# Performance work log

Hardware: AMD Instinct MI355X
Metric: run time of the kernel (lower is better)

The kernel has to match this reference:

```python
import jax, jax.numpy as jnp
import numpy as np

D = 1024   # n_embd
H = 16     # n_head
HD = D // H

def setup_inputs() -> dict:
    key = jax.random.key(0)
    ks = jax.random.split(key, 6)
    s = 1.0 / np.sqrt(D)
    x  = jax.random.normal(ks[0], (4, 2048, D), dtype=jnp.float32)
    Wq = jax.random.uniform(ks[1], (D, D), jnp.float32, -s, s)
    Wk = jax.random.uniform(ks[2], (D, D), jnp.float32, -s, s)
    Wv = jax.random.uniform(ks[3], (D, D), jnp.float32, -s, s)
    Wp = jax.random.uniform(ks[4], (D, D), jnp.float32, -s, s)
    bp = jax.random.uniform(ks[5], (D,),   jnp.float32, -s, s)
    return {"x": x, "Wq": Wq, "Wk": Wk, "Wv": Wv, "Wp": Wp, "bp": bp}

def reference(x, Wq, Wk, Wv, Wp, bp):
    B, T, C = x.shape
    scale = 1.0 / np.sqrt(HD)
    # torch nn.Linear: y = x @ W.T
    q = (x @ Wq.T).reshape(B, T, H, HD).transpose(0, 2, 1, 3)  # [B,H,T,hd]
    k = (x @ Wk.T).reshape(B, T, H, HD).transpose(0, 2, 1, 3)
    v = (x @ Wv.T).reshape(B, T, H, HD).transpose(0, 2, 1, 3)
    att = jnp.einsum('bhqd,bhkd->bhqk', q, k) * scale           # [B,H,T,T]
    causal = jnp.tril(jnp.ones((T, T), dtype=bool))
    att = jnp.where(causal[None, None], att, -jnp.inf)
    att = jax.nn.softmax(att, axis=-1)
    y = jnp.einsum('bhqk,bhkd->bhqd', att, v)                   # [B,H,T,hd]
    y = y.transpose(0, 2, 1, 3).reshape(B, T, C)
    return y @ Wp.T + bp
```

## Files before the change

kernel.cpp:

```cpp
#include <hip/hip_runtime.h>
#include <hip/hip_bf16.h>
#include <math.h>


#define B_  4
#define T_  2048
#define D_  1024
#define H_  16
#define HD_ 64
#define M_  (B_ * T_)

typedef short bf16x8 __attribute__((ext_vector_type(8)));
typedef float f32x4  __attribute__((ext_vector_type(4)));

__device__ __forceinline__ f32x4 mfma16(bf16x8 a, bf16x8 b, f32x4 c) {
    return __builtin_amdgcn_mfma_f32_16x16x32_bf16(a, b, c, 0, 0, 0);
}

__device__ __forceinline__ void gl_lds16(const unsigned short* g, unsigned short* l) {
    __builtin_amdgcn_global_load_lds(
        (const __attribute__((address_space(1))) void*)g,
        (__attribute__((address_space(3))) void*)l, 16, 0, 0);
}

__device__ __forceinline__ unsigned short f2bf(float f) {
    union { __hip_bfloat16 h; unsigned short u; } cv;
    cv.h = __float2bfloat16(f);
    return cv.u;
}
__device__ __forceinline__ float bf2f(unsigned short u) {
    return __uint_as_float(((unsigned)u) << 16);
}
__device__ __forceinline__ float exp2_fast(float x) {
    return __builtin_amdgcn_exp2f(x);
}

struct su4 { unsigned short x, y, z, w; };

__global__ __launch_bounds__(256)
void cvt_kernel(const float* __restrict__ in, unsigned short* __restrict__ out) {
    const int i = blockIdx.x * 256 + threadIdx.x;
    const float4 v = ((const float4*)in)[i];
    su4 o;
    o.x = f2bf(v.x); o.y = f2bf(v.y); o.z = f2bf(v.z); o.w = f2bf(v.w);
    ((su4*)out)[i] = o;
}

__global__ __launch_bounds__(256)
void cvtw_kernel(const float* __restrict__ w0, const float* __restrict__ w1,
                 const float* __restrict__ w2, const float* __restrict__ w3,
                 unsigned short* __restrict__ o0, unsigned short* __restrict__ o1,
                 unsigned short* __restrict__ o2, unsigned short* __restrict__ o3) {
    const int y = blockIdx.y;
    const float* in       = (y == 0) ? w0 : (y == 1) ? w1 : (y == 2) ? w2 : w3;
    unsigned short* out   = (y == 0) ? o0 : (y == 1) ? o1 : (y == 2) ? o2 : o3;
    const int i = blockIdx.x * 256 + threadIdx.x;
    const float4 v = ((const float4*)in)[i];
    su4 o;
    o.x = f2bf(v.x); o.y = f2bf(v.y); o.z = f2bf(v.z); o.w = f2bf(v.w);
    ((su4*)out)[i] = o;
}

__global__ __launch_bounds__(256, 2)
void qkv_kernel(const unsigned short* __restrict__ X,
                const unsigned short* __restrict__ Wq,
                const unsigned short* __restrict__ Wk,
                const unsigned short* __restrict__ Wv,
                unsigned short* __restrict__ Qo,
                unsigned short* __restrict__ Ko,
                unsigned short* __restrict__ Vo)
{
    __shared__ unsigned short As[128 * 64];
    __shared__ unsigned short Bs[128 * 64];

    const int m0 = blockIdx.x * 128;
    const int by = blockIdx.y;
    const unsigned short* W = (by < 8) ? Wq : (by < 16) ? Wk : Wv;
    unsigned short*       O = (by < 8) ? Qo : (by < 16) ? Ko : Vo;
    const int n0   = (by & 7) * 128;
    const bool vsec = (by >= 16);
    const int tid  = threadIdx.x;
    const int lane = tid & 63;
    const int wv   = tid >> 6;
    const int wr   = (wv >> 1) * 64;
    const int wc   = (wv & 1) * 64;
    const int g    = lane >> 4;
    const int c    = lane & 15;

    f32x4 acc[4][4] = {};

    for (int k0 = 0; k0 < D_; k0 += 64) {
        #pragma unroll
        for (int i = 0; i < 4; ++i) {
            const int flat = i * 2048 + tid * 8;
            const int row = flat >> 6, col = flat & 63;
            gl_lds16(X + (size_t)(m0 + row) * D_ + k0 + col, As + flat);
            gl_lds16(W + (size_t)(n0 + row) * D_ + k0 + col, Bs + flat);
        }
        __syncthreads();
        #pragma unroll
        for (int kk = 0; kk < 64; kk += 32) {
            bf16x8 af[4], bg[4];
            #pragma unroll
            for (int mi = 0; mi < 4; ++mi)
                af[mi] = *(const bf16x8*)(As + (wr + mi * 16 + c) * 64 + kk + g * 8);
            #pragma unroll
            for (int ni = 0; ni < 4; ++ni)
                bg[ni] = *(const bf16x8*)(Bs + (wc + ni * 16 + c) * 64 + kk + g * 8);
            if (!vsec) {
                #pragma unroll
                for (int mi = 0; mi < 4; ++mi)
                    #pragma unroll
                    for (int ni = 0; ni < 4; ++ni)
                        acc[mi][ni] = mfma16(af[mi], bg[ni], acc[mi][ni]);
            } else {
                #pragma unroll
                for (int mi = 0; mi < 4; ++mi)
                    #pragma unroll
                    for (int ni = 0; ni < 4; ++ni)
                        acc[mi][ni] = mfma16(bg[ni], af[mi], acc[mi][ni]);
            }
        }
        __syncthreads();
    }

    if (!vsec) {
        #pragma unroll
        for (int mi = 0; mi < 4; ++mi)
            #pragma unroll
            for (int ni = 0; ni < 4; ++ni)
                #pragma unroll
                for (int r = 0; r < 4; ++r) {
                    const int m = m0 + wr + mi * 16 + g * 4 + r;
                    const int n = n0 + wc + ni * 16 + c;
                    const int b = m >> 11, t = m & (T_ - 1);
                    const int h = n >> 6,  hd = n & 63;
                    O[((size_t)((b << 4) + h) * T_ + t) * HD_ + hd] = f2bf(acc[mi][ni][r]);
                }
    } else {
        #pragma unroll
        for (int mi = 0; mi < 4; ++mi)
            #pragma unroll
            for (int ni = 0; ni < 4; ++ni)
                #pragma unroll
                for (int r = 0; r < 4; ++r) {
                    const int n = n0 + wc + ni * 16 + g * 4 + r;
                    const int m = m0 + wr + mi * 16 + c;
                    const int b = m >> 11, t = m & (T_ - 1);
                    const int h = n >> 6,  hd = n & 63;
                    O[((size_t)((b << 4) + h) * HD_ + hd) * T_ + t] = f2bf(acc[mi][ni][r]);
                }
    }
}

__device__ __forceinline__ bf16x8 ptrans(const f32x4& p0, const f32x4& p1,
                                         int lane, int g, int c) {
    unsigned int P32[2][2];
    P32[0][0] = (unsigned int)f2bf(p0[0]) | ((unsigned int)f2bf(p0[1]) << 16);
    P32[0][1] = (unsigned int)f2bf(p0[2]) | ((unsigned int)f2bf(p0[3]) << 16);
    P32[1][0] = (unsigned int)f2bf(p1[0]) | ((unsigned int)f2bf(p1[1]) << 16);
    P32[1][1] = (unsigned int)f2bf(p1[2]) | ((unsigned int)f2bf(p1[3]) << 16);
    const int sl0 = c + ((lane & 16) << 1);
    const int sl1 = sl0 + 16;
    const int q00 = __shfl((int)P32[0][0], sl0), q10 = __shfl((int)P32[1][0], sl0);
    const int q01 = __shfl((int)P32[0][1], sl0), q11 = __shfl((int)P32[1][1], sl0);
    const int q02 = __shfl((int)P32[0][0], sl1), q12 = __shfl((int)P32[1][0], sl1);
    const int q03 = __shfl((int)P32[0][1], sl1), q13 = __shfl((int)P32[1][1], sl1);
    const bool nhi = (g & 2) != 0;
    union { unsigned int u[4]; bf16x8 v; } pf;
    pf.u[0] = nhi ? q10 : q00;
    pf.u[1] = nhi ? q11 : q01;
    pf.u[2] = nhi ? q12 : q02;
    pf.u[3] = nhi ? q13 : q03;
    return pf.v;
}

__global__ __launch_bounds__(256, 4)
void attn_kernel(const unsigned short* __restrict__ Q,
                 const unsigned short* __restrict__ K,
                 const unsigned short* __restrict__ VT,
                 unsigned short* __restrict__ Y)
{
    __shared__ unsigned short Ks[4096];
    __shared__ unsigned short Vs[4096];

    const int bh = blockIdx.x;
    const int pr = blockIdx.y;
    const unsigned short* Qp  = Q  + (size_t)bh * T_ * HD_;
    const unsigned short* Kp  = K  + (size_t)bh * T_ * HD_;
    const unsigned short* VTp = VT + (size_t)bh * HD_ * T_;
    const int b = bh >> 4, h = bh & 15;

    const int tid  = threadIdx.x;
    const int lane = tid & 63;
    const int w    = tid >> 6;
    const int g    = lane >> 4;
    const int c    = lane & 15;
    const float SC = 0.18033688011112042f;

    int srowK[2], scolK[2];
    #pragma unroll
    for (int i = 0; i < 2; ++i) {
        const int L = (i * 256 + tid) * 16;
        srowK[i] = L >> 7;
        scolK[i] = (L & 127) ^ ((srowK[i] & 3) << 5);
    }

    for (int hf = 0; hf < 2; ++hf) {
        const int qt = hf ? (31 - pr) : pr;
        const int qw = qt * 64 + w * 16;
        const int nt = qt + 1;

        bf16x8 qf[2];
        #pragma unroll
        for (int dk = 0; dk < 2; ++dk) {
            bf16x8 t = *(const bf16x8*)(Qp + (size_t)(qw + c) * HD_ + dk * 32 + g * 8);
            #pragma unroll
            for (int j = 0; j < 8; ++j)
                t[j] = (short)f2bf(bf2f((unsigned short)t[j]) * SC);
            qf[dk] = t;
        }

        float m_l = -1e30f, l_l = 0.f;
        f32x4 oacc[4] = {};

        for (int ti = 0; ti < nt; ++ti) {
            const int tb = ti << 6;
            const bool last = (ti == nt - 1);

            #pragma unroll
            for (int i = 0; i < 2; ++i) {
                const int L = (i * 256 + tid) * 16;
                gl_lds16(Kp + (size_t)(tb + srowK[i]) * HD_ + (scolK[i] >> 1),
                         Ks + (L >> 1));
                gl_lds16(VTp + (size_t)srowK[i] * T_ + tb + (scolK[i] >> 1),
                         Vs + (L >> 1));
            }
            __syncthreads();

            f32x4 sA[2] = {}, sB[2] = {};
            #pragma unroll
            for (int ni = 0; ni < 2; ++ni)
                #pragma unroll
                for (int dk = 0; dk < 2; ++dk) {
                    const int rA = ni * 16 + c;
                    const int rB = 32 + ni * 16 + c;
                    const bf16x8 kA = *(const bf16x8*)((const char*)Ks
                        + rA * 128 + ((dk * 64 + g * 16) ^ ((c & 3) << 5)));
                    const bf16x8 kB = *(const bf16x8*)((const char*)Ks
                        + rB * 128 + ((dk * 64 + g * 16) ^ ((c & 3) << 5)));
                    sA[ni] = mfma16(kA, qf[dk], sA[ni]);
                    sB[ni] = mfma16(kB, qf[dk], sB[ni]);
                }

            if (last) {
                #pragma unroll
                for (int ni = 0; ni < 2; ++ni)
                    #pragma unroll
                    for (int r = 0; r < 4; ++r) {
                        const int kA = tb + ni * 16 + g * 4 + r;
                        sA[ni][r] = (kA      <= qw + c) ? sA[ni][r] : -1e30f;
                        sB[ni][r] = (kA + 32 <= qw + c) ? sB[ni][r] : -1e30f;
                    }
            }

            float pmax = sA[0][0];
            #pragma unroll
            for (int ni = 0; ni < 2; ++ni)
                #pragma unroll
                for (int r = 0; r < 4; ++r) {
                    pmax = fmaxf(pmax, sA[ni][r]);
                    pmax = fmaxf(pmax, sB[ni][r]);
                }
            pmax = fmaxf(pmax, __shfl_xor(pmax, 16));
            pmax = fmaxf(pmax, __shfl_xor(pmax, 32));

            const float mn = fmaxf(m_l, pmax);
            const float al = exp2_fast(m_l - mn);
            m_l = mn;

            float rs = 0.f;
            #pragma unroll
            for (int ni = 0; ni < 2; ++ni)
                #pragma unroll
                for (int r = 0; r < 4; ++r) {
                    const float eA = exp2_fast(sA[ni][r] - mn);
                    const float eB = exp2_fast(sB[ni][r] - mn);
                    sA[ni][r] = eA; sB[ni][r] = eB;
                    rs += eA + eB;
                }
            rs += __shfl_xor(rs, 16);
            rs += __shfl_xor(rs, 32);
            l_l = l_l * al + rs;

            const bf16x8 pfA = ptrans(sA[0], sA[1], lane, g, c);
            const bf16x8 pfB = ptrans(sB[0], sB[1], lane, g, c);

            #pragma unroll
            for (int dn = 0; dn < 4; ++dn) {
                const int row = dn * 16 + c;
                const bf16x8 vA = *(const bf16x8*)((const char*)Vs
                    + row * 128 + ((g * 16)      ^ ((c & 3) << 5)));
                const bf16x8 vB = *(const bf16x8*)((const char*)Vs
                    + row * 128 + ((64 + g * 16) ^ ((c & 3) << 5)));
                #pragma unroll
                for (int r = 0; r < 4; ++r)
                    oacc[dn][r] *= al;
                oacc[dn] = mfma16(vA, pfA, oacc[dn]);
                oacc[dn] = mfma16(vB, pfB, oacc[dn]);
            }
            __syncthreads();
        }

        const float li = 1.f / l_l;
        const size_t rowoff = (size_t)(b * T_ + qw + c) * D_ + h * 64;
        #pragma unroll
        for (int dn = 0; dn < 4; ++dn) {
            const unsigned int u0 = (unsigned int)f2bf(oacc[dn][0] * li)
                                  | ((unsigned int)f2bf(oacc[dn][1] * li) << 16);
            const unsigned int u1 = (unsigned int)f2bf(oacc[dn][2] * li)
                                  | ((unsigned int)f2bf(oacc[dn][3] * li) << 16);
            uint2 st; st.x = u0; st.y = u1;
            *(uint2*)(Y + rowoff + dn * 16 + g * 4) = st;
        }
    }
}

__global__ __launch_bounds__(256, 2)
void proj_kernel(const unsigned short* __restrict__ Yin,
                 const unsigned short* __restrict__ Wp,
                 const float* __restrict__ bp,
                 float* __restrict__ Out)
{
    __shared__ unsigned short As[128 * 64];
    __shared__ unsigned short Bs[128 * 64];

    const int m0 = blockIdx.x * 128;
    const int n0 = blockIdx.y * 128;
    const int tid  = threadIdx.x;
    const int lane = tid & 63;
    const int wv   = tid >> 6;
    const int wr   = (wv >> 1) * 64;
    const int wc   = (wv & 1) * 64;
    const int g    = lane >> 4;
    const int c    = lane & 15;

    f32x4 acc[4][4] = {};

    for (int k0 = 0; k0 < D_; k0 += 64) {
        #pragma unroll
        for (int i = 0; i < 4; ++i) {
            const int flat = i * 2048 + tid * 8;
            const int row = flat >> 6, col = flat & 63;
            gl_lds16(Yin + (size_t)(m0 + row) * D_ + k0 + col, As + flat);
            gl_lds16(Wp  + (size_t)(n0 + row) * D_ + k0 + col, Bs + flat);
        }
        __syncthreads();
        #pragma unroll
        for (int kk = 0; kk < 64; kk += 32) {
            bf16x8 af[4], bg[4];
            #pragma unroll
            for (int mi = 0; mi < 4; ++mi)
                af[mi] = *(const bf16x8*)(As + (wr + mi * 16 + c) * 64 + kk + g * 8);
            #pragma unroll
            for (int ni = 0; ni < 4; ++ni)
                bg[ni] = *(const bf16x8*)(Bs + (wc + ni * 16 + c) * 64 + kk + g * 8);
            #pragma unroll
            for (int mi = 0; mi < 4; ++mi)
                #pragma unroll
                for (int ni = 0; ni < 4; ++ni)
                    acc[mi][ni] = mfma16(af[mi], bg[ni], acc[mi][ni]);
        }
        __syncthreads();
    }

    #pragma unroll
    for (int mi = 0; mi < 4; ++mi) {
        #pragma unroll
        for (int ni = 0; ni < 4; ++ni) {
            const int n = n0 + wc + ni * 16 + c;
            const float bb = bp[n];
            #pragma unroll
            for (int r = 0; r < 4; ++r) {
                const int m = m0 + wr + mi * 16 + g * 4 + r;
                Out[(size_t)m * D_ + n] = acc[mi][ni][r] + bb;
            }
        }
    }
}

extern "C" void kernel_launch(void* const* d_in, const int* in_sizes, int n_in,
                              void* d_out, int out_size, void* d_ws, size_t ws_size,
                              hipStream_t stream) {
    const float* x  = (const float*)d_in[0];
    const float* Wq = (const float*)d_in[1];
    const float* Wk = (const float*)d_in[2];
    const float* Wv = (const float*)d_in[3];
    const float* Wp = (const float*)d_in[4];
    const float* bp = (const float*)d_in[5];
    float* out = (float*)d_out;

    const size_t SZ  = (size_t)M_ * D_;
    const size_t WSZ = (size_t)D_ * D_;
    unsigned short* ws = (unsigned short*)d_ws;
    unsigned short* XB  = ws;
    unsigned short* WQB = XB  + SZ;
    unsigned short* WKB = WQB + WSZ;
    unsigned short* WVB = WKB + WSZ;
    unsigned short* WPB = WVB + WSZ;
    unsigned short* Qw  = WPB + WSZ;
    unsigned short* Kw  = Qw + SZ;
    unsigned short* Vw  = Kw + SZ;
    unsigned short* Yw  = XB;

    dim3 blk(256);
    cvt_kernel <<<dim3(SZ / 1024),     blk, 0, stream>>>(x, XB);
    cvtw_kernel<<<dim3(WSZ / 1024, 4), blk, 0, stream>>>(Wq, Wk, Wv, Wp, WQB, WKB, WVB, WPB);

    qkv_kernel <<<dim3(M_ / 128, 24), blk, 0, stream>>>(XB, WQB, WKB, WVB, Qw, Kw, Vw);
    attn_kernel<<<dim3(B_ * H_, 16), blk, 0, stream>>>(Qw, Kw, Vw, Yw);
    proj_kernel<<<dim3(M_ / 128, D_ / 128), blk, 0, stream>>>(Yw, WPB, bp, out);
}
```

Before: 208.4 us.

## Process paired causal query tiles together so each K/V tile is loaded once

The attention kernel used to handle its two query tiles (pr and 31-pr) one after the other, reloading the shared K/V tiles for each. It now runs both in a single pass over key tiles, reusing each K/V LDS tile and its K fragments for both query tiles, with the short tile masked off once it passes its diagonal. It also adds a lazy-rescale rule: the running max is left unchanged and the output rescale skipped when the new max exceeds it by at most 8 in log2 space. The cost is about twice the registers for accumulators and Q fragments, which may reduce occupancy, plus some divergent control flow.

```diff
diff --git a/kernel.cpp b/kernel.cpp
--- a/kernel.cpp
+++ b/kernel.cpp
@@ -198,128 +198,188 @@
     const int c    = lane & 15;
     const float SC = 0.18033688011112042f;
 
-    int srowK[2], scolK[2];
+    const int qtA = pr, qtB = 31 - pr;
+    const int qwA = qtA * 64 + w * 16;
+    const int qwB = qtB * 64 + w * 16;
+    const int nt  = qtB + 1;
+
+    int srow[2], scol[2];
     #pragma unroll
     for (int i = 0; i < 2; ++i) {
         const int L = (i * 256 + tid) * 16;
-        srowK[i] = L >> 7;
-        scolK[i] = (L & 127) ^ ((srowK[i] & 3) << 5);
-    }
-
-    for (int hf = 0; hf < 2; ++hf) {
-        const int qt = hf ? (31 - pr) : pr;
-        const int qw = qt * 64 + w * 16;
-        const int nt = qt + 1;
-
-        bf16x8 qf[2];
-        #pragma unroll
-        for (int dk = 0; dk < 2; ++dk) {
-            bf16x8 t = *(const bf16x8*)(Qp + (size_t)(qw + c) * HD_ + dk * 32 + g * 8);
-            #pragma unroll
-            for (int j = 0; j < 8; ++j)
-                t[j] = (short)f2bf(bf2f((unsigned short)t[j]) * SC);
-            qf[dk] = t;
-        }
-
-        float m_l = -1e30f, l_l = 0.f;
-        f32x4 oacc[4] = {};
-
-        for (int ti = 0; ti < nt; ++ti) {
-            const int tb = ti << 6;
-            const bool last = (ti == nt - 1);
-
-            #pragma unroll
-            for (int i = 0; i < 2; ++i) {
-                const int L = (i * 256 + tid) * 16;
-                gl_lds16(Kp + (size_t)(tb + srowK[i]) * HD_ + (scolK[i] >> 1),
-                         Ks + (L >> 1));
-                gl_lds16(VTp + (size_t)srowK[i] * T_ + tb + (scolK[i] >> 1),
-                         Vs + (L >> 1));
-            }
-            __syncthreads();
-
-            f32x4 sA[2] = {}, sB[2] = {};
+        srow[i] = L >> 7;
+        scol[i] = (L & 127) ^ ((srow[i] & 3) << 5);
+    }
+
+    bf16x8 qfA[2], qfB[2];
+    #pragma unroll
+    for (int dk = 0; dk < 2; ++dk) {
+        bf16x8 tA = *(const bf16x8*)(Qp + (size_t)(qwA + c) * HD_ + dk * 32 + g * 8);
+        bf16x8 tB = *(const bf16x8*)(Qp + (size_t)(qwB + c) * HD_ + dk * 32 + g * 8);
+        #pragma unroll
+        for (int j = 0; j < 8; ++j) {
+            tA[j] = (short)f2bf(bf2f((unsigned short)tA[j]) * SC);
+            tB[j] = (short)f2bf(bf2f((unsigned short)tB[j]) * SC);
+        }
+        qfA[dk] = tA;
+        qfB[dk] = tB;
+    }
+
+    float mA = -1e30f, lA = 0.f, mB = -1e30f, lB = 0.f;
+    f32x4 oA[4] = {}, oB[4] = {};
+
+    auto softmax64 = [&](f32x4 (&s0)[2], f32x4 (&s1)[2], int tb, int qw, bool last,
+                         float& m_l, float& l_l, float& al_out, bool& skip_out) {
+        if (last) {
             #pragma unroll
             for (int ni = 0; ni < 2; ++ni)
                 #pragma unroll
+                for (int r = 0; r < 4; ++r) {
+                    const int kA = tb + ni * 16 + g * 4 + r;
+                    s0[ni][r] = (kA      <= qw + c) ? s0[ni][r] : -1e30f;
+                    s1[ni][r] = (kA + 32 <= qw + c) ? s1[ni][r] : -1e30f;
+                }
+        }
+        float pmax = s0[0][0];
+        #pragma unroll
+        for (int ni = 0; ni < 2; ++ni)
+            #pragma unroll
+            for (int r = 0; r < 4; ++r) {
+                pmax = fmaxf(pmax, s0[ni][r]);
+                pmax = fmaxf(pmax, s1[ni][r]);
+            }
+        pmax = fmaxf(pmax, __shfl_xor(pmax, 16));
+        pmax = fmaxf(pmax, __shfl_xor(pmax, 32));
+
+        const bool skip = __all(pmax - m_l <= 8.0f);
+        float al = 1.f;
+        if (!skip) {
+            const float mn = fmaxf(m_l, pmax);
+            al = exp2_fast(m_l - mn);
+            m_l = mn;
+        }
+        float rs = 0.f;
+        #pragma unroll
+        for (int ni = 0; ni < 2; ++ni)
+            #pragma unroll
+            for (int r = 0; r < 4; ++r) {
+                const float e0 = exp2_fast(s0[ni][r] - m_l);
+                const float e1 = exp2_fast(s1[ni][r] - m_l);
+                s0[ni][r] = e0; s1[ni][r] = e1;
+                rs += e0 + e1;
+            }
+        rs += __shfl_xor(rs, 16);
+        rs += __shfl_xor(rs, 32);
+        l_l = l_l * al + rs;
+        al_out = al;
+        skip_out = skip;
+    };
+
+    for (int ti = 0; ti < nt; ++ti) {
+        const int tb = ti << 6;
+        const bool actA = (ti <= qtA);
+
+        #pragma unroll
+        for (int i = 0; i < 2; ++i) {
+            const int L = (i * 256 + tid) * 16;
+            gl_lds16(Kp + (size_t)(tb + srow[i]) * HD_ + (scol[i] >> 1),
+                     Ks + (L >> 1));
+            gl_lds16(VTp + (size_t)srow[i] * T_ + tb + (scol[i] >> 1),
+                     Vs + (L >> 1));
+        }
+        __syncthreads();
+
+        bf16x8 kf[8];
+        #pragma unroll
+        for (int s = 0; s < 2; ++s)
+            #pragma unroll
+            for (int ni = 0; ni < 2; ++ni)
+                #pragma unroll
+                for (int dk = 0; dk < 2; ++dk)
+                    kf[s * 4 + ni * 2 + dk] = *(const bf16x8*)((const char*)Ks
+                        + (s * 32 + ni * 16 + c) * 128
+                        + ((dk * 64 + g * 16) ^ ((c & 3) << 5)));
+
+        f32x4 sB0[2] = {}, sB1[2] = {};
+        f32x4 sA0[2] = {}, sA1[2] = {};
+        #pragma unroll
+        for (int ni = 0; ni < 2; ++ni)
+            #pragma unroll
+            for (int dk = 0; dk < 2; ++dk) {
+                sB0[ni] = mfma16(kf[ni * 2 + dk],     qfB[dk], sB0[ni]);
+                sB1[ni] = mfma16(kf[4 + ni * 2 + dk], qfB[dk], sB1[ni]);
+            }
+        if (actA) {
+            #pragma unroll
+            for (int ni = 0; ni < 2; ++ni)
+                #pragma unroll
                 for (int dk = 0; dk < 2; ++dk) {
-                    const int rA = ni * 16 + c;
-                    const int rB = 32 + ni * 16 + c;
-                    const bf16x8 kA = *(const bf16x8*)((const char*)Ks
-                        + rA * 128 + ((dk * 64 + g * 16) ^ ((c & 3) << 5)));
-                    const bf16x8 kB = *(const bf16x8*)((const char*)Ks
-                        + rB * 128 + ((dk * 64 + g * 16) ^ ((c & 3) << 5)));
-                    sA[ni] = mfma16(kA, qf[dk], sA[ni]);
-                    sB[ni] = mfma16(kB, qf[dk], sB[ni]);
+                    sA0[ni] = mfma16(kf[ni * 2 + dk],     qfA[dk], sA0[ni]);
+                    sA1[ni] = mfma16(kf[4 + ni * 2 + dk], qfA[dk], sA1[ni]);
                 }
-
-            if (last) {
-                #pragma unroll
-                for (int ni = 0; ni < 2; ++ni)
+        }
+
+        float alB, alA = 1.f;
+        bool skB, skA = true;
+        softmax64(sB0, sB1, tb, qwB, ti == qtB, mB, lB, alB, skB);
+        const bf16x8 pfB0 = ptrans(sB0[0], sB0[1], lane, g, c);
+        const bf16x8 pfB1 = ptrans(sB1[0], sB1[1], lane, g, c);
+        bf16x8 pfA0, pfA1;
+        if (actA) {
+            softmax64(sA0, sA1, tb, qwA, ti == qtA, mA, lA, alA, skA);
+            pfA0 = ptrans(sA0[0], sA0[1], lane, g, c);
+            pfA1 = ptrans(sA1[0], sA1[1], lane, g, c);
+        }
+
+        #pragma unroll
+        for (int dn = 0; dn < 4; ++dn) {
+            const int row = dn * 16 + c;
+            const bf16x8 vA = *(const bf16x8*)((const char*)Vs
+                + row * 128 + ((g * 16)      ^ ((c & 3) << 5)));
+            const bf16x8 vB = *(const bf16x8*)((const char*)Vs
+                + row * 128 + ((64 + g * 16) ^ ((c & 3) << 5)));
+            if (!skB) {
+                #pragma unroll
+                for (int r = 0; r < 4; ++r)
+                    oB[dn][r] *= alB;
+            }
+            oB[dn] = mfma16(vA, pfB0, oB[dn]);
+            oB[dn] = mfma16(vB, pfB1, oB[dn]);
+            if (actA) {
+                if (!skA) {
                     #pragma unroll
-                    for (int r = 0; r < 4; ++r) {
-                        const int kA = tb + ni * 16 + g * 4 + r;
-                        sA[ni][r] = (kA      <= qw + c) ? sA[ni][r] : -1e30f;
-                        sB[ni][r] = (kA + 32 <= qw + c) ? sB[ni][r] : -1e30f;
-                    }
-            }
-
-            float pmax = sA[0][0];
-            #pragma unroll
-            for (int ni = 0; ni < 2; ++ni)
-                #pragma unroll
-                for (int r = 0; r < 4; ++r) {
-                    pmax = fmaxf(pmax, sA[ni][r]);
-                    pmax = fmaxf(pmax, sB[ni][r]);
+                    for (int r = 0; r < 4; ++r)
+                        oA[dn][r] *= alA;
                 }
-            pmax = fmaxf(pmax, __shfl_xor(pmax, 16));
-            pmax = fmaxf(pmax, __shfl_xor(pmax, 32));
-
-            const float mn = fmaxf(m_l, pmax);
-            const float al = exp2_fast(m_l - mn);
-            m_l = mn;
-
-            float rs = 0.f;
-            #pragma unroll
-            for (int ni = 0; ni < 2; ++ni)
-                #pragma unroll
-                for (int r = 0; r < 4; ++r) {
-                    const float eA = exp2_fast(sA[ni][r] - mn);
-                    const float eB = exp2_fast(sB[ni][r] - mn);
-                    sA[ni][r] = eA; sB[ni][r] = eB;
-                    rs += eA + eB;
-                }
-            rs += __shfl_xor(rs, 16);
-            rs += __shfl_xor(rs, 32);
-            l_l = l_l * al + rs;
-
-            const bf16x8 pfA = ptrans(sA[0], sA[1], lane, g, c);
-            const bf16x8 pfB = ptrans(sB[0], sB[1], lane, g, c);
-
-            #pragma unroll
-            for (int dn = 0; dn < 4; ++dn) {
-                const int row = dn * 16 + c;
-                const bf16x8 vA = *(const bf16x8*)((const char*)Vs
-                    + row * 128 + ((g * 16)      ^ ((c & 3) << 5)));
-                const bf16x8 vB = *(const bf16x8*)((const char*)Vs
-                    + row * 128 + ((64 + g * 16) ^ ((c & 3) << 5)));
-                #pragma unroll
-                for (int r = 0; r < 4; ++r)
-                    oacc[dn][r] *= al;
-                oacc[dn] = mfma16(vA, pfA, oacc[dn]);
-                oacc[dn] = mfma16(vB, pfB, oacc[dn]);
-            }
-            __syncthreads();
-        }
-
-        const float li = 1.f / l_l;
-        const size_t rowoff = (size_t)(b * T_ + qw + c) * D_ + h * 64;
+                oA[dn] = mfma16(vA, pfA0, oA[dn]);
+                oA[dn] = mfma16(vB, pfA1, oA[dn]);
+            }
+        }
+        __syncthreads();
+    }
+
+    {
+        const float li = 1.f / lA;
+        const size_t rowoff = (size_t)(b * T_ + qwA + c) * D_ + h * 64;
         #pragma unroll
         for (int dn = 0; dn < 4; ++dn) {
-            const unsigned int u0 = (unsigned int)f2bf(oacc[dn][0] * li)
-                                  | ((unsigned int)f2bf(oacc[dn][1] * li) << 16);
-            const unsigned int u1 = (unsigned int)f2bf(oacc[dn][2] * li)
-                                  | ((unsigned int)f2bf(oacc[dn][3] * li) << 16);
+            const unsigned int u0 = (unsigned int)f2bf(oA[dn][0] * li)
+                                  | ((unsigned int)f2bf(oA[dn][1] * li) << 16);
+            const unsigned int u1 = (unsigned int)f2bf(oA[dn][2] * li)
+                                  | ((unsigned int)f2bf(oA[dn][3] * li) << 16);
+            uint2 st; st.x = u0; st.y = u1;
+            *(uint2*)(Y + rowoff + dn * 16 + g * 4) = st;
+        }
+    }
+    {
+        const float li = 1.f / lB;
+        const size_t rowoff = (size_t)(b * T_ + qwB + c) * D_ + h * 64;
+        #pragma unroll
+        for (int dn = 0; dn < 4; ++dn) {
+            const unsigned int u0 = (unsigned int)f2bf(oB[dn][0] * li)
+                                  | ((unsigned int)f2bf(oB[dn][1] * li) << 16);
+            const unsigned int u1 = (unsigned int)f2bf(oB[dn][2] * li)
+                                  | ((unsigned int)f2bf(oB[dn][3] * li) << 16);
             uint2 st; st.x = u0; st.y = u1;
             *(uint2*)(Y + rowoff + dn * 16 + g * 4) = st;
         }
```

New measurement: 228.0 us. 1.09x slower.
